# Performance work log

Hardware: AMD Instinct MI355X
Metric: run time of the kernel (lower is better)

## Reference

```python
import jax, jax.numpy as jnp
import numpy as np

EPS_DIR = 1e-15
EPS_W = 1e-5
NEAR_MIN = 0.05


def setup_inputs() -> dict:
    key = jax.random.key(0)
    k1, k2, k3 = jax.random.split(key, 3)
    B, N, T = 1, 262144, 128
    rays_o = jax.random.normal(k1, (B, N, 3), dtype=jnp.float32)
    rays_d = jax.random.normal(k2, (B, N, 3), dtype=jnp.float32)
    weights = jax.random.uniform(k3, (B * N, T - 1), dtype=jnp.float32)
    return {"rays_o": rays_o, "rays_d": rays_d, "weights": weights,
            "bound": 1, "n_samples": 128}


def _near_far_cube(ro, rd, bound):
    # ro, rd: [R, 3]
    tmin = (-bound - ro) / (rd + EPS_DIR)
    tmax = (bound - ro) / (rd + EPS_DIR)
    near = jnp.max(jnp.minimum(tmin, tmax), axis=-1, keepdims=True)  # [R,1]
    far = jnp.min(jnp.maximum(tmin, tmax), axis=-1, keepdims=True)   # [R,1]
    near = jnp.maximum(near, NEAR_MIN)
    return near, far


def _sample_pdf(bins, weights, n_samples):
    # bins: [R, T], weights: [R, T-1]; deterministic (det=True) inverse-CDF sampling
    w = weights + EPS_W
    pdf = w / jnp.sum(w, axis=-1, keepdims=True)
    cdf = jnp.cumsum(pdf, axis=-1)
    cdf = jnp.concatenate([jnp.zeros_like(cdf[..., :1]), cdf], axis=-1)  # [R, T]
    n = n_samples
    u = jnp.linspace(0.5 / n, 1.0 - 0.5 / n, n, dtype=cdf.dtype)
    u = jnp.broadcast_to(u, cdf.shape[:-1] + (n,))                        # [R, n]
    inds = jax.vmap(lambda c, uu: jnp.searchsorted(c, uu, side='right'))(cdf, u)
    T = cdf.shape[-1]
    below = jnp.maximum(inds - 1, 0)
    above = jnp.minimum(inds, T - 1)
    cdf_lo = jnp.take_along_axis(cdf, below, axis=-1)
    cdf_hi = jnp.take_along_axis(cdf, above, axis=-1)
    bin_lo = jnp.take_along_axis(bins, below, axis=-1)
    bin_hi = jnp.take_along_axis(bins, above, axis=-1)
    denom = cdf_hi - cdf_lo
    denom = jnp.where(denom < EPS_W, jnp.ones_like(denom), denom)
    t = (u - cdf_lo) / denom
    return bin_lo + t * (bin_hi - bin_lo)  # [R, n]


def reference(rays_o, rays_d, weights, bound, n_samples):
    ro = rays_o.reshape(-1, 3)
    rd = rays_d.reshape(-1, 3)
    near, far = _near_far_cube(ro, rd, float(bound))          # [R,1]
    T = weights.shape[-1] + 1
    z = jnp.linspace(0.0, 1.0, T, dtype=ro.dtype)[None, :]    # [1,T]
    z_vals = near + (far - near) * z                          # [R,T] coarse bins
    new_z_vals = _sample_pdf(z_vals, weights, n_samples)      # [R,n_samples]
    return new_z_vals
```

## Files before the change

### kernel.cpp

```cpp
#include <hip/hip_runtime.h>

#define EPS_DIR 1e-15f
#define EPS_W   1e-5f
#define NEAR_MIN 0.05f

__global__ __launch_bounds__(256) void nerf_sample_pdf_kernel(
    const float* __restrict__ rays_o,
    const float* __restrict__ rays_d,
    const float* __restrict__ weights,
    const int*   __restrict__ bound_p,
    float*       __restrict__ out,
    int R, int Tm1, int n)
{
    const int lane = threadIdx.x & 63;
    const int wid  = threadIdx.x >> 6;
    const int ray  = blockIdx.x * 4 + wid;
    if (ray >= R) return;

    const float* wrow = weights + (size_t)ray * Tm1;
    const int i0 = 2 * lane, i1 = 2 * lane + 1;
    float w0 = (i0 < Tm1) ? (wrow[i0] + EPS_W) : 0.0f;
    float w1 = (i1 < Tm1) ? (wrow[i1] + EPS_W) : 0.0f;
    const float local = w0 + w1;

    float S = local;
#pragma unroll
    for (int off = 1; off < 64; off <<= 1) {
        float y = __shfl_up(S, off, 64);
        if (lane >= off) S += y;
    }
    const float total = __shfl(S, 63, 64);
    const float rinv  = __builtin_amdgcn_rcpf(total);

    float prevS = __shfl_up(S, 1, 64);
    if (lane == 0) prevS = 0.0f;

    const float c_lo  = prevS * rinv;
    const float c_hi  = S * rinv;
    const float c_mid = (prevS + w0) * rinv;

    const float b = (float)bound_p[0];
    float nearv = -3.4e38f, farv = 3.4e38f;
#pragma unroll
    for (int k = 0; k < 3; ++k) {
        float o = rays_o[(size_t)ray * 3 + k];
        float d = rays_d[(size_t)ray * 3 + k] + EPS_DIR;
        float r = __builtin_amdgcn_rcpf(d);
        float t0 = (-b - o) * r;
        float t1 = ( b - o) * r;
        nearv = fmaxf(nearv, fminf(t0, t1));
        farv  = fminf(farv,  fmaxf(t0, t1));
    }
    nearv = fmaxf(nearv, NEAR_MIN);

    const float scale = (farv - nearv) * __builtin_amdgcn_rcpf((float)Tm1);
    const float d0 = c_mid - c_lo;
    const float d1 = c_hi - c_mid;
    const float rden0 = (d0 < EPS_W) ? 1.0f : __builtin_amdgcn_rcpf(d0);
    const float rden1 = (d1 < EPS_W) ? 1.0f : __builtin_amdgcn_rcpf(d1);
    const float zb0 = nearv + scale * (float)i0;
    const float zb1 = zb0 + scale;

    const float fn    = (float)n;
    const float inv_n = 1.0f / fn;

    int j0 = (int)ceilf(fn * c_lo - 0.5f);
    if (j0 < 0) j0 = 0;
    int j1;
    const bool last = (i1 >= Tm1 - 1);
    if (last) {
        j1 = n;
    } else {
        j1 = (int)ceilf(fn * c_hi - 0.5f);
        if (j1 > n) j1 = n;
    }

    float* __restrict__ orow = out + (size_t)ray * n;
    for (int j = j0; j < j1; ++j) {
        float u = ((float)j + 0.5f) * inv_n;
        bool second = (u >= c_mid) && (i1 < Tm1);
        float lo  = second ? c_mid : c_lo;
        float rd  = second ? rden1 : rden0;
        float zb  = second ? zb1   : zb0;
        float t   = (u - lo) * rd;
        orow[j] = fmaf(t, scale, zb);
    }
}

extern "C" void kernel_launch(void* const* d_in, const int* in_sizes, int n_in,
                              void* d_out, int out_size, void* d_ws, size_t ws_size,
                              hipStream_t stream) {
    const float* rays_o  = (const float*)d_in[0];
    const float* rays_d  = (const float*)d_in[1];
    const float* weights = (const float*)d_in[2];
    const int*   bound_p = (const int*)d_in[3];
    float*       out     = (float*)d_out;

    const int R   = in_sizes[0] / 3;
    const int Tm1 = in_sizes[2] / R;
    const int n   = out_size / R;

    dim3 grid((R + 3) / 4), block(256);
    nerf_sample_pdf_kernel<<<grid, block, 0, stream>>>(
        rays_o, rays_d, weights, bound_p, out, R, Tm1, n);
}
```

Baseline: 284.5 us.

## Switch from one wavefront per ray to one thread per ray with sequential merge

The kernel previously mapped each ray to a 64-lane wavefront that did a shuffle-based prefix scan and had each lane write its own output range. Now each thread handles a whole ray: it sums the weight row serially, then walks the CDF and the sample positions together in a merge loop, writing the results as float4. This removes the shuffle scan and the divergent per-lane store loops. In exchange, each thread reads its row with a stride of Tm1 floats, so global loads and stores are no longer coalesced across the wavefront, and the data-dependent while loop can diverge between lanes.

```diff
diff --git a/kernel.cpp b/kernel.cpp
--- a/kernel.cpp
+++ b/kernel.cpp
@@ -12,32 +12,8 @@
     float*       __restrict__ out,
     int R, int Tm1, int n)
 {
-    const int lane = threadIdx.x & 63;
-    const int wid  = threadIdx.x >> 6;
-    const int ray  = blockIdx.x * 4 + wid;
+    const int ray = blockIdx.x * blockDim.x + threadIdx.x;
     if (ray >= R) return;
-
-    const float* wrow = weights + (size_t)ray * Tm1;
-    const int i0 = 2 * lane, i1 = 2 * lane + 1;
-    float w0 = (i0 < Tm1) ? (wrow[i0] + EPS_W) : 0.0f;
-    float w1 = (i1 < Tm1) ? (wrow[i1] + EPS_W) : 0.0f;
-    const float local = w0 + w1;
-
-    float S = local;
-#pragma unroll
-    for (int off = 1; off < 64; off <<= 1) {
-        float y = __shfl_up(S, off, 64);
-        if (lane >= off) S += y;
-    }
-    const float total = __shfl(S, 63, 64);
-    const float rinv  = __builtin_amdgcn_rcpf(total);
-
-    float prevS = __shfl_up(S, 1, 64);
-    if (lane == 0) prevS = 0.0f;
-
-    const float c_lo  = prevS * rinv;
-    const float c_hi  = S * rinv;
-    const float c_mid = (prevS + w0) * rinv;
 
     const float b = (float)bound_p[0];
     float nearv = -3.4e38f, farv = 3.4e38f;
@@ -52,38 +28,68 @@
         farv  = fminf(farv,  fmaxf(t0, t1));
     }
     nearv = fmaxf(nearv, NEAR_MIN);
+    const float scale = (farv - nearv) * __builtin_amdgcn_rcpf((float)Tm1);
 
-    const float scale = (farv - nearv) * __builtin_amdgcn_rcpf((float)Tm1);
-    const float d0 = c_mid - c_lo;
-    const float d1 = c_hi - c_mid;
-    const float rden0 = (d0 < EPS_W) ? 1.0f : __builtin_amdgcn_rcpf(d0);
-    const float rden1 = (d1 < EPS_W) ? 1.0f : __builtin_amdgcn_rcpf(d1);
-    const float zb0 = nearv + scale * (float)i0;
-    const float zb1 = zb0 + scale;
+    const float* __restrict__ wrow = weights + (size_t)ray * Tm1;
 
-    const float fn    = (float)n;
-    const float inv_n = 1.0f / fn;
+    float s0 = 0.f, s1 = 0.f, s2 = 0.f, s3 = 0.f;
+    int i = 0;
+    for (; i + 4 <= Tm1; i += 4) {
+        s0 += wrow[i + 0];
+        s1 += wrow[i + 1];
+        s2 += wrow[i + 2];
+        s3 += wrow[i + 3];
+    }
+    for (; i < Tm1; ++i) s0 += wrow[i];
+    const float total = ((s0 + s1) + (s2 + s3)) + (float)Tm1 * EPS_W;
+    const float rtot  = __builtin_amdgcn_rcpf(total);
 
-    int j0 = (int)ceilf(fn * c_lo - 0.5f);
-    if (j0 < 0) j0 = 0;
-    int j1;
-    const bool last = (i1 >= Tm1 - 1);
-    if (last) {
-        j1 = n;
-    } else {
-        j1 = (int)ceilf(fn * c_hi - 0.5f);
-        if (j1 > n) j1 = n;
-    }
+    const float inv_n = 1.0f / (float)n;
+    float u    = 0.5f * inv_n;
+    int   idx  = 0;
+    float c_lo = 0.0f;
+    float c_hi = (wrow[0] + EPS_W) * rtot;
+    float wnext = (Tm1 > 1) ? wrow[1] : 0.0f;
+    const int last = Tm1 - 1;
 
     float* __restrict__ orow = out + (size_t)ray * n;
-    for (int j = j0; j < j1; ++j) {
-        float u = ((float)j + 0.5f) * inv_n;
-        bool second = (u >= c_mid) && (i1 < Tm1);
-        float lo  = second ? c_mid : c_lo;
-        float rd  = second ? rden1 : rden0;
-        float zb  = second ? zb1   : zb0;
-        float t   = (u - lo) * rd;
-        orow[j] = fmaf(t, scale, zb);
+
+    const int ng = n >> 2;
+    for (int g = 0; g < ng; ++g) {
+        float z0, z1, z2, z3;
+#pragma unroll
+        for (int s = 0; s < 4; ++s) {
+            while (c_hi <= u && idx < last) {
+                ++idx;
+                c_lo = c_hi;
+                const float wn = wnext + EPS_W;
+                wnext = wrow[(idx + 1 < Tm1) ? (idx + 1) : last];
+                c_hi  = c_lo + wn * rtot;
+            }
+            const float d  = c_hi - c_lo;
+            const float rd = (d < EPS_W) ? 1.0f : __builtin_amdgcn_rcpf(d);
+            const float t  = (u - c_lo) * rd;
+            const float z  = fmaf(scale, (float)idx + t, nearv);
+            if      (s == 0) z0 = z;
+            else if (s == 1) z1 = z;
+            else if (s == 2) z2 = z;
+            else             z3 = z;
+            u += inv_n;
+        }
+        *reinterpret_cast<float4*>(orow + 4 * g) = make_float4(z0, z1, z2, z3);
+    }
+    for (int j = ng * 4; j < n; ++j) {
+        while (c_hi <= u && idx < last) {
+            ++idx;
+            c_lo = c_hi;
+            const float wn = wnext + EPS_W;
+            wnext = wrow[(idx + 1 < Tm1) ? (idx + 1) : last];
+            c_hi  = c_lo + wn * rtot;
+        }
+        const float d  = c_hi - c_lo;
+        const float rd = (d < EPS_W) ? 1.0f : __builtin_amdgcn_rcpf(d);
+        orow[j] = fmaf(scale, (float)idx + (u - c_lo) * rd, nearv);
+        u += inv_n;
     }
 }
 
@@ -100,7 +106,7 @@
     const int Tm1 = in_sizes[2] / R;
     const int n   = out_size / R;
 
-    dim3 grid((R + 3) / 4), block(256);
+    dim3 grid((R + 255) / 256), block(256);
     nerf_sample_pdf_kernel<<<grid, block, 0, stream>>>(
         rays_o, rays_d, weights, bound_p, out, R, Tm1, n);
 }
```

Result: slower. 809.9 us (+184.7%).

## Replace per-bin sample loops with per-sample binary search over shared-memory CDF

Applied to the files above, without the earlier changes.

Each wave now writes its ray's CDF into LDS, and each lane binary-searches it for two output samples. Before, each lane looped over the samples falling into its own bin, which gave divergent, uneven loops and scattered scalar stores. The new layout gives every lane equal work and writes coalesced float2 stores. In exchange it adds LDS traffic, a block-wide barrier, and seven search steps per sample.

```diff
diff --git a/kernel.cpp b/kernel.cpp
--- a/kernel.cpp
+++ b/kernel.cpp
@@ -14,16 +14,19 @@
 {
     const int lane = threadIdx.x & 63;
     const int wid  = threadIdx.x >> 6;
-    const int ray  = blockIdx.x * 4 + wid;
-    if (ray >= R) return;
+    int ray = blockIdx.x * 4 + wid;
+    const bool valid = (ray < R);
+    if (!valid) ray = R - 1;
 
-    const float* wrow = weights + (size_t)ray * Tm1;
+    __shared__ float cdf_s[4][132];
+    float* __restrict__ cdf = cdf_s[wid];
+
+    const float* __restrict__ wrow = weights + (size_t)ray * Tm1;
     const int i0 = 2 * lane, i1 = 2 * lane + 1;
     float w0 = (i0 < Tm1) ? (wrow[i0] + EPS_W) : 0.0f;
     float w1 = (i1 < Tm1) ? (wrow[i1] + EPS_W) : 0.0f;
-    const float local = w0 + w1;
 
-    float S = local;
+    float S = w0 + w1;
 #pragma unroll
     for (int off = 1; off < 64; off <<= 1) {
         float y = __shfl_up(S, off, 64);
@@ -31,13 +34,12 @@
     }
     const float total = __shfl(S, 63, 64);
     const float rinv  = __builtin_amdgcn_rcpf(total);
-
     float prevS = __shfl_up(S, 1, 64);
     if (lane == 0) prevS = 0.0f;
 
-    const float c_lo  = prevS * rinv;
-    const float c_hi  = S * rinv;
-    const float c_mid = (prevS + w0) * rinv;
+    cdf[i0] = prevS * rinv;
+    cdf[i1] = (prevS + w0) * rinv;
+    __syncthreads();
 
     const float b = (float)bound_p[0];
     float nearv = -3.4e38f, farv = 3.4e38f;
@@ -52,38 +54,44 @@
         farv  = fminf(farv,  fmaxf(t0, t1));
     }
     nearv = fmaxf(nearv, NEAR_MIN);
-
     const float scale = (farv - nearv) * __builtin_amdgcn_rcpf((float)Tm1);
-    const float d0 = c_mid - c_lo;
-    const float d1 = c_hi - c_mid;
-    const float rden0 = (d0 < EPS_W) ? 1.0f : __builtin_amdgcn_rcpf(d0);
-    const float rden1 = (d1 < EPS_W) ? 1.0f : __builtin_amdgcn_rcpf(d1);
-    const float zb0 = nearv + scale * (float)i0;
-    const float zb1 = zb0 + scale;
-
-    const float fn    = (float)n;
-    const float inv_n = 1.0f / fn;
-
-    int j0 = (int)ceilf(fn * c_lo - 0.5f);
-    if (j0 < 0) j0 = 0;
-    int j1;
-    const bool last = (i1 >= Tm1 - 1);
-    if (last) {
-        j1 = n;
-    } else {
-        j1 = (int)ceilf(fn * c_hi - 0.5f);
-        if (j1 > n) j1 = n;
-    }
+    const float inv_n = 1.0f / (float)n;
 
     float* __restrict__ orow = out + (size_t)ray * n;
-    for (int j = j0; j < j1; ++j) {
-        float u = ((float)j + 0.5f) * inv_n;
-        bool second = (u >= c_mid) && (i1 < Tm1);
-        float lo  = second ? c_mid : c_lo;
-        float rd  = second ? rden1 : rden0;
-        float zb  = second ? zb1   : zb0;
-        float t   = (u - lo) * rd;
-        orow[j] = fmaf(t, scale, zb);
+
+    for (int base = 0; base < n; base += 128) {
+        const int j = base + 2 * lane;
+        if (j >= n) break;
+        const float u0 = ((float)j + 0.5f) * inv_n;
+        const float u1 = u0 + inv_n;
+
+        int   p0 = 0,   p1 = 0;
+        float v0 = 0.f, v1 = 0.f;
+#pragma unroll
+        for (int step = 64; step >= 1; step >>= 1) {
+            const float c0 = cdf[p0 + step];
+            const float c1 = cdf[p1 + step];
+            if (c0 <= u0) { p0 += step; v0 = c0; }
+            if (c1 <= u1) { p1 += step; v1 = c1; }
+        }
+        const int a0 = (p0 < Tm1) ? p0 + 1 : Tm1;
+        const int a1 = (p1 < Tm1) ? p1 + 1 : Tm1;
+        const float h0 = cdf[a0];
+        const float h1 = cdf[a1];
+        const float d0 = h0 - v0;
+        const float d1 = h1 - v1;
+        const float t0 = (u0 - v0) * ((d0 < EPS_W) ? 1.0f : __builtin_amdgcn_rcpf(d0));
+        const float t1 = (u1 - v1) * ((d1 < EPS_W) ? 1.0f : __builtin_amdgcn_rcpf(d1));
+        const float z0 = fmaf(t0, (float)(a0 - p0) * scale, fmaf((float)p0, scale, nearv));
+        const float z1 = fmaf(t1, (float)(a1 - p1) * scale, fmaf((float)p1, scale, nearv));
+
+        if (valid) {
+            if (j + 1 < n) {
+                *reinterpret_cast<float2*>(orow + j) = make_float2(z0, z1);
+            } else {
+                orow[j] = z0;
+            }
+        }
     }
 }
 
```

New measurement: 295.4 us. 1.04x slower.
